# Performance work log

Hardware: AMD Instinct MI355X
Metric: run time of the kernel (lower is better)

Reference implementation:

```python
import jax, jax.numpy as jnp
import numpy as np

B, S, DIN, DH, DOUT = 8, 2048, 512, 1024, 16


def setup_inputs() -> dict:
    key = jax.random.key(0)
    ks = jax.random.split(key, 7)
    x = jax.random.normal(ks[0], (B, S, DIN), dtype=jnp.float32)
    # MLP params (Linear stores W as [in, out] here; we apply x @ W + b)
    w1 = jax.random.normal(ks[1], (DIN, DH), dtype=jnp.float32) / np.sqrt(DIN)
    b1 = jnp.zeros((DH,), dtype=jnp.float32)
    w2 = jax.random.normal(ks[2], (DH, DH), dtype=jnp.float32) / np.sqrt(DH)
    b2 = jnp.zeros((DH,), dtype=jnp.float32)
    w3 = jax.random.normal(ks[3], (DH, DOUT), dtype=jnp.float32) / np.sqrt(DH)
    b3 = jnp.zeros((DOUT,), dtype=jnp.float32)
    # decay buffer: exact dyadics 1 - 2^-(c+3), matches init_kwargs list
    decay = 1.0 - 2.0 ** (-(jnp.arange(DOUT, dtype=jnp.float32) + 3.0))
    # D[i, t, c] = decay_c^(t - i) for t >= i else 0 (upper triangular per channel)
    idx = jnp.arange(S)
    exps = idx[None, :] - idx[:, None]            # [S, S], t - i
    mask = (exps >= 0).astype(jnp.float32)        # triu mask
    exps_c = jnp.maximum(exps, 0).astype(jnp.float32)
    D = mask[:, :, None] * (decay[None, None, :] ** exps_c[:, :, None])  # [S, S, DOUT]
    return {"input_temporal": x, "w1": w1, "b1": b1, "w2": w2, "b2": b2,
            "w3": w3, "b3": b3, "D": D}


def reference(input_temporal, w1, b1, w2, b2, w3, b3, D):
    # 3-layer MLP (dropout=0 -> identity in eval)
    h = jax.nn.relu(input_temporal @ w1 + b1)
    h = jax.nn.relu(h @ w2 + b2)
    o = h @ w3 + b3                               # [B, S, DOUT]
    # decay-weighted causal mixing: out[b,t,c] = sum_{i<=t} o[b,i,c] * decay_c^(t-i)
    # (equivalent to torch repeat+multiply+sum, without materializing [B,S,S,D])
    mixed = jnp.einsum('bic,itc->btc', o, D)
    # extra running cumsum as in the original forward
    return jnp.cumsum(mixed, axis=1)
```

## Files before the change

### kernel.cpp

```cpp
#include <hip/hip_runtime.h>

typedef unsigned int u32;
typedef unsigned short u16;
typedef float f32x4 __attribute__((ext_vector_type(4)));
typedef short bf16x8 __attribute__((ext_vector_type(8)));

__device__ __forceinline__ u16 f2bf(float f) {
  u32 u = __builtin_bit_cast(u32, f);
  u += 0x7FFFu + ((u >> 16) & 1u);
  return (u16)(u >> 16);
}
__device__ __forceinline__ void gload_lds16(const void* g, void* l) {
  __builtin_amdgcn_global_load_lds(
      (const __attribute__((address_space(1))) void*)g,
      (__attribute__((address_space(3))) void*)l, 16, 0, 0);
}

__global__ __launch_bounds__(256) void prep_k(
    const float* __restrict__ x, uint2* __restrict__ A1,
    const float* __restrict__ w1, u16* __restrict__ w1t,
    const float* __restrict__ w2, u16* __restrict__ w2t,
    const float* __restrict__ w3, u16* __restrict__ w3t) {
  const int bid = blockIdx.x;
  const int tid = threadIdx.x;
  if (bid >= 3072) {
    int i = (bid - 3072) * 256 + tid;
    float4 v = ((const float4*)x)[i];
    uint2 o;
    o.x = (u32)f2bf(v.x) | ((u32)f2bf(v.y) << 16);
    o.y = (u32)f2bf(v.z) | ((u32)f2bf(v.w) << 16);
    A1[i] = o;
    return;
  }
  __shared__ float tile[32][33];
  const int z = bid >> 10, t = bid & 1023;
  const int bx = t & 31, by = t >> 5;
  const float* in; u16* out; int R, C;
  if (z == 0)      { in = w1; out = w1t; R = 512;  C = 1024; }
  else if (z == 1) { in = w2; out = w2t; R = 1024; C = 1024; }
  else             { in = w3; out = w3t; R = 1024; C = 16;   }
  int c0 = bx * 32, r0 = by * 32;
  if (c0 >= C || r0 >= R) return;
  int tx = tid & 31, ty = tid >> 5;
  #pragma unroll
  for (int j = 0; j < 4; j++) {
    int r = r0 + ty + j * 8, c = c0 + tx;
    if (r < R && c < C) tile[ty + j * 8][tx] = in[(size_t)r * C + c];
  }
  __syncthreads();
  #pragma unroll
  for (int j = 0; j < 4; j++) {
    int c = c0 + ty + j * 8, r = r0 + tx;
    if (r < R && c < C) out[(size_t)c * R + r] = f2bf(tile[tx][ty + j * 8]);
  }
}

__global__ __launch_bounds__(512, 2) void gemm1d_k(
    const u16* __restrict__ A, const u16* __restrict__ Bt,
    const float* __restrict__ bias, u16* __restrict__ C,
    int M, int N, int K) {
  __shared__ __align__(16) char lds[4 * 32768];
  const int tid = threadIdx.x;
  const int rr = blockIdx.x;
  const int xcd = rr & 7, sid = rr >> 3;
  const int bm = (xcd << 3) | (sid >> 2);
  const int bnp = sid & 3;
  const int wave = tid >> 6, lane = tid & 63;
  const int wm = wave >> 1, wn = wave & 1;
  const int l15 = lane & 15, l4 = lane >> 4;
  const int NT = K >> 5;
  const size_t arow0 = (size_t)bm * 256, brow0 = (size_t)bnp * 256;

  f32x4 acc[2][4][4];
  #pragma unroll
  for (int h = 0; h < 2; h++)
    #pragma unroll
    for (int m = 0; m < 4; m++)
      #pragma unroll
      for (int n = 0; n < 4; n++) acc[h][m][n] = (f32x4){0.f, 0.f, 0.f, 0.f};

  auto stage = [&](int kt, int s) {
    char* sA = lds + s * 32768;
    char* sB = sA + 16384;
    #pragma unroll
    for (int j = 0; j < 2; j++) {
      int ch = tid + j * 512;
      int row = ch >> 2;
      int col4 = (ch & 3) ^ (row & 3);
      gload_lds16(A + (arow0 + row) * K + kt * 32 + col4 * 8, sA + ch * 16);
    }
    #pragma unroll
    for (int j = 0; j < 2; j++) {
      int ch = tid + j * 512;
      int row = ch >> 2;
      int col4 = (ch & 3) ^ (row & 3);
      gload_lds16(Bt + (brow0 + row) * K + kt * 32 + col4 * 8, sB + ch * 16);
    }
  };

  stage(0, 0);
  stage(1, 1);
  stage(2, 2);
  asm volatile("s_waitcnt vmcnt(8)" ::: "memory");
  __builtin_amdgcn_s_barrier();

  for (int t = 0; t < NT; t++) {
    const int s = t & 3;
    const char* sA = lds + s * 32768;
    const char* sB = sA + 16384;

    bf16x8 af[4];
    #pragma unroll
    for (int m = 0; m < 4; m++) {
      int r = wm * 64 + m * 16 + l15;
      af[m] = *(const bf16x8*)(sA + r * 64 + ((l4 ^ (r & 3)) << 4));
    }
    bf16x8 b0[4];
    #pragma unroll
    for (int n = 0; n < 4; n++) {
      int r = wn * 64 + n * 16 + l15;
      b0[n] = *(const bf16x8*)(sB + r * 64 + ((l4 ^ (r & 3)) << 4));
    }
    if (t + 3 < NT) stage(t + 3, (t + 3) & 3);

    __builtin_amdgcn_s_barrier();
    asm volatile("s_waitcnt lgkmcnt(0)" ::: "memory");
    __builtin_amdgcn_sched_barrier(0);
    __builtin_amdgcn_s_setprio(1);
    #pragma unroll
    for (int m = 0; m < 4; m++)
      #pragma unroll
      for (int n = 0; n < 4; n++)
        acc[0][m][n] = __builtin_amdgcn_mfma_f32_16x16x32_bf16(
            af[m], b0[n], acc[0][m][n], 0, 0, 0);
    __builtin_amdgcn_s_setprio(0);

    bf16x8 b1[4];
    #pragma unroll
    for (int n = 0; n < 4; n++) {
      int r = 128 + wn * 64 + n * 16 + l15;
      b1[n] = *(const bf16x8*)(sB + r * 64 + ((l4 ^ (r & 3)) << 4));
    }
    __builtin_amdgcn_s_barrier();
    asm volatile("s_waitcnt lgkmcnt(0)" ::: "memory");
    __builtin_amdgcn_sched_barrier(0);
    __builtin_amdgcn_s_setprio(1);
    #pragma unroll
    for (int m = 0; m < 4; m++)
      #pragma unroll
      for (int n = 0; n < 4; n++)
        acc[1][m][n] = __builtin_amdgcn_mfma_f32_16x16x32_bf16(
            af[m], b1[n], acc[1][m][n], 0, 0, 0);
    __builtin_amdgcn_s_setprio(0);

    if (t + 1 < NT) {
      if (t + 3 < NT)
        asm volatile("s_waitcnt vmcnt(8)" ::: "memory");
      else if (t + 2 < NT)
        asm volatile("s_waitcnt vmcnt(4)" ::: "memory");
      else
        asm volatile("s_waitcnt vmcnt(0)" ::: "memory");
      __builtin_amdgcn_s_barrier();
    }
  }

  #pragma unroll
  for (int h = 0; h < 2; h++) {
    int bn = bnp * 2 + h;
    #pragma unroll
    for (int n = 0; n < 4; n++) {
      int col = bn * 128 + wn * 64 + n * 16 + l15;
      float bv = bias[col];
      #pragma unroll
      for (int m = 0; m < 4; m++) {
        int row0 = bm * 256 + wm * 64 + m * 16 + l4 * 4;
        #pragma unroll
        for (int r = 0; r < 4; r++) {
          float v = acc[h][m][n][r] + bv;
          v = v > 0.f ? v : 0.f;
          C[(size_t)(row0 + r) * N + col] = f2bf(v);
        }
      }
    }
  }
}

__global__ __launch_bounds__(512, 2) void gemm2f_k(
    const u16* __restrict__ A, const u16* __restrict__ Bt,
    const float* __restrict__ bias, const u16* __restrict__ w3t,
    float* __restrict__ part, int M, int N, int K) {
  __shared__ __align__(16) char lds[131072];
  const int tid = threadIdx.x;
  const int rr = blockIdx.x;
  const int xcd = rr & 7, slot_id = rr >> 3;
  const int bm = (xcd << 3) | (slot_id >> 2);
  const int bn = slot_id & 3;
  const int wave = tid >> 6, lane = tid & 63;
  const int wm = wave >> 2, wn = wave & 3;
  const int l15 = lane & 15, l4 = lane >> 4;
  const int NT = K >> 5;
  const size_t arow0 = (size_t)bm * 256, brow0 = (size_t)bn * 256;

  f32x4 acc[4][8];
  #pragma unroll
  for (int p = 0; p < 4; p++)
    #pragma unroll
    for (int q = 0; q < 8; q++) acc[p][q] = (f32x4){0.f, 0.f, 0.f, 0.f};

  auto stage = [&](int kt, int s) {
    char* sA = lds + s * 32768;
    char* sB = sA + 16384;
    #pragma unroll
    for (int j = 0; j < 2; j++) {
      int ch = tid + j * 512;
      int row = ch >> 2;
      int col4 = (ch & 3) ^ (row & 3);
      gload_lds16(A + (arow0 + row) * K + kt * 32 + col4 * 8, sA + ch * 16);
    }
    #pragma unroll
    for (int j = 0; j < 2; j++) {
      int ch = tid + j * 512;
      int row = ch >> 2;
      int col4 = (ch & 3) ^ (row & 3);
      gload_lds16(Bt + (brow0 + row) * K + kt * 32 + col4 * 8, sB + ch * 16);
    }
  };

  stage(0, 0);
  stage(1, 1);
  stage(2, 2);
  asm volatile("s_waitcnt vmcnt(8)" ::: "memory");
  __builtin_amdgcn_s_barrier();

  for (int t = 0; t < NT; t++) {
    const int s = t & 3;
    const char* sA = lds + s * 32768;
    const char* sB = sA + 16384;

    bf16x8 bfr[4];
    #pragma unroll
    for (int n = 0; n < 4; n++) {
      int r = wn * 64 + n * 16 + l15;
      bfr[n] = *(const bf16x8*)(sB + r * 64 + ((l4 ^ (r & 3)) << 4));
    }
    bf16x8 af0[4];
    #pragma unroll
    for (int m = 0; m < 4; m++) {
      int r = wm * 128 + m * 16 + l15;
      af0[m] = *(const bf16x8*)(sA + r * 64 + ((l4 ^ (r & 3)) << 4));
    }
    if (t + 3 < NT) stage(t + 3, (t + 3) & 3);

    __builtin_amdgcn_s_barrier();
    asm volatile("s_waitcnt lgkmcnt(0)" ::: "memory");
    __builtin_amdgcn_sched_barrier(0);
    __builtin_amdgcn_s_setprio(1);
    #pragma unroll
    for (int p = 0; p < 4; p++)
      #pragma unroll
      for (int q = 0; q < 4; q++)
        acc[p][q] = __builtin_amdgcn_mfma_f32_16x16x32_bf16(
            bfr[p], af0[q], acc[p][q], 0, 0, 0);
    __builtin_amdgcn_s_setprio(0);

    bf16x8 af1[4];
    #pragma unroll
    for (int m = 0; m < 4; m++) {
      int r = wm * 128 + (m + 4) * 16 + l15;
      af1[m] = *(const bf16x8*)(sA + r * 64 + ((l4 ^ (r & 3)) << 4));
    }
    __builtin_amdgcn_s_barrier();
    asm volatile("s_waitcnt lgkmcnt(0)" ::: "memory");
    __builtin_amdgcn_sched_barrier(0);
    __builtin_amdgcn_s_setprio(1);
    #pragma unroll
    for (int p = 0; p < 4; p++)
      #pragma unroll
      for (int q = 0; q < 4; q++)
        acc[p][q + 4] = __builtin_amdgcn_mfma_f32_16x16x32_bf16(
            bfr[p], af1[q], acc[p][q + 4], 0, 0, 0);
    __builtin_amdgcn_s_setprio(0);

    if (t + 1 < NT) {
      if (t + 3 < NT)
        asm volatile("s_waitcnt vmcnt(8)" ::: "memory");
      else if (t + 2 < NT)
        asm volatile("s_waitcnt vmcnt(4)" ::: "memory");
      else
        asm volatile("s_waitcnt vmcnt(0)" ::: "memory");
      __builtin_amdgcn_s_barrier();
    }
  }

  __builtin_amdgcn_s_barrier();
  #pragma unroll
  for (int p = 0; p < 4; p++) {
    float4 bv = *(const float4*)(bias + wn * 64 + p * 16 + l4 * 4);
    int colb = (wn * 64 + p * 16 + l4 * 4) * 2;
    #pragma unroll
    for (int q = 0; q < 8; q++) {
      int hrow = wm * 128 + q * 16 + l15;
      float v0 = acc[p][q][0] + bv.x; v0 = v0 > 0.f ? v0 : 0.f;
      float v1 = acc[p][q][1] + bv.y; v1 = v1 > 0.f ? v1 : 0.f;
      float v2 = acc[p][q][2] + bv.z; v2 = v2 > 0.f ? v2 : 0.f;
      float v3 = acc[p][q][3] + bv.w; v3 = v3 > 0.f ? v3 : 0.f;
      uint2 pk;
      pk.x = (u32)f2bf(v0) | ((u32)f2bf(v1) << 16);
      pk.y = (u32)f2bf(v2) | ((u32)f2bf(v3) << 16);
      *(uint2*)(lds + hrow * 512 + (colb ^ ((hrow & 7) << 4))) = pk;
    }
  }
  __builtin_amdgcn_s_barrier();

  bf16x8 wf[8];
  {
    const u16* w3row = w3t + (size_t)l15 * 1024 + bn * 256 + l4 * 8;
    #pragma unroll
    for (int kk = 0; kk < 8; kk++)
      wf[kk] = *(const bf16x8*)(w3row + kk * 32);
  }
  #pragma unroll
  for (int g = 0; g < 2; g++) {
    int row0 = wave * 32 + g * 16;
    int row = row0 + l15;
    f32x4 oacc = (f32x4){0.f, 0.f, 0.f, 0.f};
    #pragma unroll
    for (int kk = 0; kk < 8; kk++) {
      bf16x8 hf = *(const bf16x8*)(lds + row * 512 +
                                   ((kk * 64 + l4 * 16) ^ ((row & 7) << 4)));
      oacc = __builtin_amdgcn_mfma_f32_16x16x32_bf16(hf, wf[kk], oacc,
                                                     0, 0, 0);
    }
    int grow = bm * 256 + row0 + l4 * 4;
    int b = grow >> 11, s = grow & 2047;
    float4 st = {oacc[0], oacc[1], oacc[2], oacc[3]};
    *(float4*)(part + ((size_t)bn * 128 + b * 16 + l15) * 2048 + s) = st;
  }
}

__global__ __launch_bounds__(64) void scan_k(
    const float* __restrict__ part, const float* __restrict__ b3,
    float* __restrict__ out) {
  const int chain = blockIdx.x;
  const int lane = threadIdx.x;
  const int b = chain >> 4, c = chain & 15;
  const float dinv = __builtin_bit_cast(float, (u32)((127 - (c + 3)) << 23));
  const float d = 1.f - dinv;
  const float b3c = b3[c];

  float o[32];
  #pragma unroll
  for (int i = 0; i < 8; i++) {
    float4 acc4 = {b3c, b3c, b3c, b3c};
    #pragma unroll
    for (int p = 0; p < 4; p++) {
      const float4* src = (const float4*)(part + (size_t)p * 262144 +
                                          (size_t)chain * 2048 + lane * 32);
      float4 v = src[i];
      acc4.x += v.x; acc4.y += v.y; acc4.z += v.z; acc4.w += v.w;
    }
    o[i * 4 + 0] = acc4.x; o[i * 4 + 1] = acc4.y;
    o[i * 4 + 2] = acc4.z; o[i * 4 + 3] = acc4.w;
  }

  float M = 0.f, A = 0.f, P = 1.f, S = 0.f;
  #pragma unroll
  for (int i = 0; i < 32; i++) {
    M = d * M + o[i];
    A += M;
    P *= d;
    S = d * S + d;
  }

  #pragma unroll
  for (int off = 1; off < 64; off <<= 1) {
    float Pp = __shfl_up(P, off, 64);
    float Mp = __shfl_up(M, off, 64);
    float Sp = __shfl_up(S, off, 64);
    float Ap = __shfl_up(A, off, 64);
    if (lane >= off) {
      float A2 = Ap + S * Mp + A;
      float S2 = Sp + S * Pp;
      float M2 = P * Mp + M;
      float P2 = Pp * P;
      A = A2; S = S2; M = M2; P = P2;
    }
  }
  float m0 = __shfl_up(M, 1, 64);
  float a0 = __shfl_up(A, 1, 64);
  if (lane == 0) { m0 = 0.f; a0 = 0.f; }

  float* dst = out + (size_t)b * 32768 + (size_t)(lane * 32) * 16 + c;
  float m = m0, a = a0;
  #pragma unroll
  for (int i = 0; i < 32; i++) {
    m = d * m + o[i];
    a += m;
    dst[i * 16] = a;
  }
}

extern "C" void kernel_launch(void* const* d_in, const int* in_sizes, int n_in,
                              void* d_out, int out_size, void* d_ws, size_t ws_size,
                              hipStream_t stream) {
  const float* x  = (const float*)d_in[0];
  const float* w1 = (const float*)d_in[1];
  const float* b1 = (const float*)d_in[2];
  const float* w2 = (const float*)d_in[3];
  const float* b2 = (const float*)d_in[4];
  const float* w3 = (const float*)d_in[5];
  const float* b3 = (const float*)d_in[6];
  float* out = (float*)d_out;

  char* ws = (char*)d_ws;
  size_t off = 0;
  u16* A1   = (u16*)(ws + off); off += (size_t)16384 * 512 * 2;
  u16* h1   = (u16*)(ws + off); off += (size_t)16384 * 1024 * 2;
  u16* w1t  = (u16*)(ws + off); off += (size_t)1024 * 512 * 2;
  u16* w2t  = (u16*)(ws + off); off += (size_t)1024 * 1024 * 2;
  u16* w3t  = (u16*)(ws + off); off += (size_t)16 * 1024 * 2;
  float* part = (float*)(ws + off); off += (size_t)4 * 128 * 2048 * 4;

  prep_k<<<11264, 256, 0, stream>>>(x, (uint2*)A1, w1, w1t, w2, w2t, w3, w3t);
  gemm1d_k<<<256, 512, 0, stream>>>(A1, w1t, b1, h1, 16384, 1024, 512);
  gemm2f_k<<<256, 512, 0, stream>>>(h1, w2t, b2, w3t, part,
                                    16384, 1024, 1024);
  scan_k<<<128, 64, 0, stream>>>(part, b3, out);
}
```

Baseline: 82.00 us.

## Fuse fp32-to-bf16 conversion of x into first GEMM's LDS load path

The separate prep pass that converted x to bf16 into a workspace buffer is dropped. The first GEMM now streams fp32 x directly into LDS with an 8-way swizzle and converts to bf16 in registers with packed cvt instructions before the MFMAs. This removes a full read and write of x plus the reread of the bf16 copy. In exchange the A tile doubles in LDS size, so the pipeline drops from four stages to three (prefetch depth 2), and each step now carries extra conversion ALU work and twice the A load bandwidth.

```diff
diff --git a/kernel.cpp b/kernel.cpp
--- a/kernel.cpp
+++ b/kernel.cpp
@@ -15,23 +15,18 @@
       (const __attribute__((address_space(1))) void*)g,
       (__attribute__((address_space(3))) void*)l, 16, 0, 0);
 }
+__device__ __forceinline__ u32 cvtpk_bf16(float lo, float hi) {
+  u32 r;
+  asm("v_cvt_pk_bf16_f32 %0, %1, %2" : "=v"(r) : "v"(lo), "v"(hi));
+  return r;
+}
 
 __global__ __launch_bounds__(256) void prep_k(
-    const float* __restrict__ x, uint2* __restrict__ A1,
     const float* __restrict__ w1, u16* __restrict__ w1t,
     const float* __restrict__ w2, u16* __restrict__ w2t,
     const float* __restrict__ w3, u16* __restrict__ w3t) {
   const int bid = blockIdx.x;
   const int tid = threadIdx.x;
-  if (bid >= 3072) {
-    int i = (bid - 3072) * 256 + tid;
-    float4 v = ((const float4*)x)[i];
-    uint2 o;
-    o.x = (u32)f2bf(v.x) | ((u32)f2bf(v.y) << 16);
-    o.y = (u32)f2bf(v.z) | ((u32)f2bf(v.w) << 16);
-    A1[i] = o;
-    return;
-  }
   __shared__ float tile[32][33];
   const int z = bid >> 10, t = bid & 1023;
   const int bx = t & 31, by = t >> 5;
@@ -56,10 +51,10 @@
 }
 
 __global__ __launch_bounds__(512, 2) void gemm1d_k(
-    const u16* __restrict__ A, const u16* __restrict__ Bt,
+    const float* __restrict__ X, const u16* __restrict__ Bt,
     const float* __restrict__ bias, u16* __restrict__ C,
     int M, int N, int K) {
-  __shared__ __align__(16) char lds[4 * 32768];
+  __shared__ __align__(16) char lds[3 * 49152];
   const int tid = threadIdx.x;
   const int rr = blockIdx.x;
   const int xcd = rr & 7, sid = rr >> 3;
@@ -80,14 +75,14 @@
       for (int n = 0; n < 4; n++) acc[h][m][n] = (f32x4){0.f, 0.f, 0.f, 0.f};
 
   auto stage = [&](int kt, int s) {
-    char* sA = lds + s * 32768;
-    char* sB = sA + 16384;
-    #pragma unroll
-    for (int j = 0; j < 2; j++) {
+    char* sA = lds + s * 49152;
+    char* sB = sA + 32768;
+    #pragma unroll
+    for (int j = 0; j < 4; j++) {
       int ch = tid + j * 512;
-      int row = ch >> 2;
-      int col4 = (ch & 3) ^ (row & 3);
-      gload_lds16(A + (arow0 + row) * K + kt * 32 + col4 * 8, sA + ch * 16);
+      int row = ch >> 3;
+      int g = (ch & 7) ^ (row & 7);
+      gload_lds16(X + (arow0 + row) * K + kt * 32 + g * 4, sA + ch * 16);
     }
     #pragma unroll
     for (int j = 0; j < 2; j++) {
@@ -100,20 +95,23 @@
 
   stage(0, 0);
   stage(1, 1);
-  stage(2, 2);
-  asm volatile("s_waitcnt vmcnt(8)" ::: "memory");
+  asm volatile("s_waitcnt vmcnt(6)" ::: "memory");
   __builtin_amdgcn_s_barrier();
 
   for (int t = 0; t < NT; t++) {
-    const int s = t & 3;
-    const char* sA = lds + s * 32768;
-    const char* sB = sA + 16384;
+    const int s = t % 3;
+    const char* sA = lds + s * 49152;
+    const char* sB = sA + 32768;
 
     bf16x8 af[4];
     #pragma unroll
     for (int m = 0; m < 4; m++) {
       int r = wm * 64 + m * 16 + l15;
-      af[m] = *(const bf16x8*)(sA + r * 64 + ((l4 ^ (r & 3)) << 4));
+      f32x4 a0 = *(const f32x4*)(sA + r * 128 + ((((l4 << 1)) ^ (r & 7)) << 4));
+      f32x4 a1 = *(const f32x4*)(sA + r * 128 + ((((l4 << 1) | 1) ^ (r & 7)) << 4));
+      uint4 pk = {cvtpk_bf16(a0[0], a0[1]), cvtpk_bf16(a0[2], a0[3]),
+                  cvtpk_bf16(a1[0], a1[1]), cvtpk_bf16(a1[2], a1[3])};
+      af[m] = __builtin_bit_cast(bf16x8, pk);
     }
     bf16x8 b0[4];
     #pragma unroll
@@ -121,7 +119,7 @@
       int r = wn * 64 + n * 16 + l15;
       b0[n] = *(const bf16x8*)(sB + r * 64 + ((l4 ^ (r & 3)) << 4));
     }
-    if (t + 3 < NT) stage(t + 3, (t + 3) & 3);
+    if (t + 2 < NT) stage(t + 2, (t + 2) % 3);
 
     __builtin_amdgcn_s_barrier();
     asm volatile("s_waitcnt lgkmcnt(0)" ::: "memory");
@@ -154,10 +152,8 @@
     __builtin_amdgcn_s_setprio(0);
 
     if (t + 1 < NT) {
-      if (t + 3 < NT)
-        asm volatile("s_waitcnt vmcnt(8)" ::: "memory");
-      else if (t + 2 < NT)
-        asm volatile("s_waitcnt vmcnt(4)" ::: "memory");
+      if (t + 2 < NT)
+        asm volatile("s_waitcnt vmcnt(6)" ::: "memory");
       else
         asm volatile("s_waitcnt vmcnt(0)" ::: "memory");
       __builtin_amdgcn_s_barrier();
@@ -414,15 +410,14 @@
 
   char* ws = (char*)d_ws;
   size_t off = 0;
-  u16* A1   = (u16*)(ws + off); off += (size_t)16384 * 512 * 2;
   u16* h1   = (u16*)(ws + off); off += (size_t)16384 * 1024 * 2;
   u16* w1t  = (u16*)(ws + off); off += (size_t)1024 * 512 * 2;
   u16* w2t  = (u16*)(ws + off); off += (size_t)1024 * 1024 * 2;
   u16* w3t  = (u16*)(ws + off); off += (size_t)16 * 1024 * 2;
   float* part = (float*)(ws + off); off += (size_t)4 * 128 * 2048 * 4;
 
-  prep_k<<<11264, 256, 0, stream>>>(x, (uint2*)A1, w1, w1t, w2, w2t, w3, w3t);
-  gemm1d_k<<<256, 512, 0, stream>>>(A1, w1t, b1, h1, 16384, 1024, 512);
+  prep_k<<<3072, 256, 0, stream>>>(w1, w1t, w2, w2t, w3, w3t);
+  gemm1d_k<<<256, 512, 0, stream>>>(x, w1t, b1, h1, 16384, 1024, 512);
   gemm2f_k<<<256, 512, 0, stream>>>(h1, w2t, b2, w3t, part,
                                     16384, 1024, 1024);
   scan_k<<<128, 64, 0, stream>>>(part, b3, out);
```

Measured after the change: 80.31 us. 1.02x faster.
